# Optimization experiments

Hardware: AMD Instinct MI355X
Metric: run time of the kernel (lower is better)

Reference implementation:

```python
import jax, jax.numpy as jnp
import numpy as np

EPS = 1e-12  # F.normalize default eps

def _l2norm(v):
    # torch F.normalize: v / max(||v||, eps)
    n = jnp.sqrt(jnp.sum(v * v, axis=-1, keepdims=True))
    return v / jnp.maximum(n, EPS)

def setup_inputs() -> dict:
    key = jax.random.key(0)
    k1, k2, k3 = jax.random.split(key, 3)
    bn, cn, d = 8192, 16384, 512
    x = jax.random.normal(k1, (bn, d), dtype=jnp.float32)
    positive = jax.random.normal(k2, (bn, d), dtype=jnp.float32)
    negative = jax.random.normal(k3, (cn, d), dtype=jnp.float32)
    return {"x": x, "positive": positive, "negative": negative}

def reference(x, positive, negative):
    # normalize x and positive explicitly (as in the torch code);
    # cosine_similarity(x_n, negative) == x_n @ normalize(negative).T since x_n is unit-norm
    xn = _l2norm(x)            # (bn, d)
    pn = _l2norm(positive)     # (bn, d)
    nn_ = _l2norm(negative)    # (cn, d)
    sim = jnp.sum(xn * pn, axis=1)                 # (bn,) positive cosine sim
    logits = jnp.einsum('bd,cd->bc', xn, nn_)      # (bn, cn) cosine sims vs negatives
    denom = jnp.sum(jnp.exp(logits), axis=1)       # (bn,) -- logits bounded in [-1,1], safe
    bn = x.shape[0]
    loss = -jnp.sum(sim - jnp.log(denom)) / bn
    return loss
```

## Files before the change

kernel.cpp:

```cpp
#include <hip/hip_runtime.h>
#include <stdint.h>

#define D 512
#define BNROWS 8192
#define CNROWS 16384
#define NPART 256

typedef __attribute__((ext_vector_type(4))) float f32x4;
typedef __attribute__((ext_vector_type(8))) __bf16 bf16x8;
typedef __attribute__((ext_vector_type(8))) short s16x8;

typedef const __attribute__((address_space(1))) unsigned int* gas_ptr;
typedef __attribute__((address_space(3))) unsigned int* las_ptr;

__device__ __forceinline__ void gload_lds16(const void* g, void* l) {
    __builtin_amdgcn_global_load_lds((gas_ptr)g, (las_ptr)l, 16, 0, 0);
}

__device__ __forceinline__ short f2bf(float f) {
    uint32_t u = __float_as_uint(f);
    uint32_t r = (u + 0x7FFFu + ((u >> 16) & 1u)) >> 16;
    return (short)r;
}

__device__ __forceinline__ float wave_reduce_add(float v) {
#pragma unroll
    for (int m = 32; m >= 1; m >>= 1) v += __shfl_xor(v, m, 64);
    return v;
}

__global__ __launch_bounds__(256) void k_norm(const float* __restrict__ x,
                                              const float* __restrict__ p,
                                              const float* __restrict__ n,
                                              short* __restrict__ xnb,
                                              short* __restrict__ nnb,
                                              float* __restrict__ sim) {
    const int wid = threadIdx.x >> 6, lane = threadIdx.x & 63;
    if (blockIdx.x < BNROWS / 4) {
        const int row = blockIdx.x * 4 + wid;
        const float* xr = x + (size_t)row * D + lane * 8;
        const float* pr = p + (size_t)row * D + lane * 8;
        f32x4 x0 = *(const f32x4*)xr, x1 = *(const f32x4*)(xr + 4);
        f32x4 p0 = *(const f32x4*)pr, p1 = *(const f32x4*)(pr + 4);
        float xx = 0.f, pp = 0.f, xp = 0.f;
#pragma unroll
        for (int j = 0; j < 4; ++j) {
            xx += x0[j] * x0[j] + x1[j] * x1[j];
            pp += p0[j] * p0[j] + p1[j] * p1[j];
            xp += x0[j] * p0[j] + x1[j] * p1[j];
        }
        xx = wave_reduce_add(xx);
        pp = wave_reduce_add(pp);
        xp = wave_reduce_add(xp);
        const float rx = 1.0f / fmaxf(sqrtf(xx), 1e-12f);
        const float rp = 1.0f / fmaxf(sqrtf(pp), 1e-12f);
        if (lane == 0) sim[row] = xp * rx * rp;
        s16x8 o;
#pragma unroll
        for (int j = 0; j < 4; ++j) {
            o[j] = f2bf(x0[j] * rx);
            o[j + 4] = f2bf(x1[j] * rx);
        }
        *(s16x8*)(xnb + (size_t)row * D + lane * 8) = o;
    } else {
        const int row = (blockIdx.x - BNROWS / 4) * 4 + wid;
        const float* nr = n + (size_t)row * D + lane * 8;
        f32x4 n0 = *(const f32x4*)nr, n1 = *(const f32x4*)(nr + 4);
        float nn = 0.f;
#pragma unroll
        for (int j = 0; j < 4; ++j) nn += n0[j] * n0[j] + n1[j] * n1[j];
        nn = wave_reduce_add(nn);
        const float rn = 1.0f / fmaxf(sqrtf(nn), 1e-12f);
        s16x8 o;
#pragma unroll
        for (int j = 0; j < 4; ++j) {
            o[j] = f2bf(n0[j] * rn);
            o[j + 4] = f2bf(n1[j] * rn);
        }
        *(s16x8*)(nnb + (size_t)row * D + lane * 8) = o;
    }
}


#define LOAD_A(buf, mh)                                                                  \
    {                                                                                    \
        _Pragma("unroll") for (int m2 = 0; m2 < 4; ++m2) _Pragma("unroll") for (int ks = \
                                                                                    0;   \
                                                                                ks < 2;  \
                                                                                ++ks)    \
            af[m2 * 2 + ks] =                                                            \
            *(const bf16x8*)(Ard[buf] + (mh)*512 + m2 * 128 + ks * 4096);                \
    }
#define LOAD_B(buf, nh)                                                                  \
    {                                                                                    \
        _Pragma("unroll") for (int n2 = 0; n2 < 2; ++n2) _Pragma("unroll") for (int ks = \
                                                                                    0;   \
                                                                                ks < 2;  \
                                                                                ++ks)    \
            bfr[((nh)*2 + n2) * 2 + ks] =                                                \
            *(const bf16x8*)(Brd[buf] + ((nh)*2 + n2) * 128 + ks * 4096);                \
    }
#define MMA(mh, nh)                                                                     \
    {                                                                                   \
        _Pragma("unroll") for (int m2 = 0; m2 < 4; ++m2)                                \
            _Pragma("unroll") for (int n2 = 0; n2 < 2; ++n2)                            \
                _Pragma("unroll") for (int ks = 0; ks < 2; ++ks) acc[(mh)*4 + m2]       \
                                                                   [(nh)*2 + n2] =     \
                __builtin_amdgcn_mfma_f32_16x16x32_bf16(af[m2 * 2 + ks],                \
                                                        bfr[((nh)*2 + n2) * 2 + ks],   \
                                                        acc[(mh)*4 + m2][(nh)*2 + n2], \
                                                        0, 0, 0);                      \
    }
#define STAGE_A(buf, h, kt)                                      \
    {                                                            \
        gload_lds16(agp[h] + (kt)*64, dstA[buf][h]);             \
        gload_lds16(agp[h] + (kt)*64 + 32, dstA[buf][h] + 4096); \
    }
#define STAGE_B(buf, h, kt)                                      \
    {                                                            \
        gload_lds16(bgp[h] + (kt)*64, dstB[buf][h]);             \
        gload_lds16(bgp[h] + (kt)*64 + 32, dstB[buf][h] + 4096); \
    }
#define BAR() __builtin_amdgcn_s_barrier()
#define LGKM0() asm volatile("s_waitcnt lgkmcnt(0)" ::: "memory")
#define PRIO1() __builtin_amdgcn_s_setprio(1)
#define PRIO0() __builtin_amdgcn_s_setprio(0)
#define VMC4() asm volatile("s_waitcnt vmcnt(4)" ::: "memory")
#define VMC0() asm volatile("s_waitcnt vmcnt(0)" ::: "memory")

#define ITER(t0, ST)                                                                 \
    {                                                                                \
         LOAD_A(0, 0); LOAD_B(0, 0); STAGE_A(1, 0, (t0) + 1);                  \
        BAR(); LGKM0(); PRIO1(); MMA(0, 0); PRIO0(); BAR();                          \
         LOAD_B(0, 1); STAGE_A(1, 1, (t0) + 1);                                \
        BAR(); LGKM0(); PRIO1(); MMA(0, 1); PRIO0(); BAR();                          \
         LOAD_A(0, 1); if (ST) STAGE_B(0, 0, (t0) + 2);                        \
        BAR(); LGKM0(); PRIO1(); MMA(1, 0); PRIO0(); BAR();                          \
         if (ST) STAGE_B(0, 1, (t0) + 2);                                      \
        BAR(); PRIO1(); MMA(1, 1); PRIO0();                                          \
        if (ST) VMC4(); else VMC0();                                                 \
        BAR();                                                                       \
         LOAD_A(1, 0); LOAD_B(1, 0); if (ST) STAGE_A(0, 0, (t0) + 2);          \
        BAR(); LGKM0(); PRIO1(); MMA(0, 0); PRIO0(); BAR();                          \
         LOAD_B(1, 1); if (ST) STAGE_A(0, 1, (t0) + 2);                        \
        BAR(); LGKM0(); PRIO1(); MMA(0, 1); PRIO0(); BAR();                          \
         LOAD_A(1, 1); if (ST) STAGE_B(1, 0, (t0) + 3);                        \
        BAR(); LGKM0(); PRIO1(); MMA(1, 0); PRIO0(); BAR();                          \
         if (ST) STAGE_B(1, 1, (t0) + 3);                                      \
        BAR(); PRIO1(); MMA(1, 1); PRIO0();                                          \
        if (ST) VMC4();                                                              \
        BAR();                                                                       \
    }

__global__ __launch_bounds__(512, 2) void k_gemm_exp(const short* __restrict__ A,
                                                     const short* __restrict__ B,
                                                     float* __restrict__ part) {
    __shared__ short lds[2][2][2][8][128][8];

    const int t = threadIdx.x;
    const int lane = t & 63, wid = t >> 6;
    const int wr = wid >> 2, wc = wid & 3;
    const int lg = lane >> 4, lm = lane & 15;
    const int blockM = blockIdx.y * 256;
    const int blockN = blockIdx.x * 256;

    const int row_s = t & 127, kg_s = t >> 7;
    const short* agp[2];
    const short* bgp[2];
    short* dstA[2][2];
    short* dstB[2][2];
#pragma unroll
    for (int h = 0; h < 2; ++h) {
        agp[h] = A + (size_t)(blockM + h * 128 + row_s) * D + kg_s * 8;
        bgp[h] = B + (size_t)(blockN + h * 128 + row_s) * D + kg_s * 8;
#pragma unroll
        for (int buf = 0; buf < 2; ++buf) {
            dstA[buf][h] = &lds[buf][0][h][kg_s][row_s][0];
            dstB[buf][h] = &lds[buf][1][h][kg_s][row_s][0];
        }
    }
    const short* Ard[2];
    const short* Brd[2];
#pragma unroll
    for (int buf = 0; buf < 2; ++buf) {
        Ard[buf] = &lds[buf][0][wr][lg][lm][0];
        Brd[buf] = &lds[buf][1][wc >> 1][lg][(wc & 1) * 64 + lm][0];
    }

    f32x4 acc[8][4];
#pragma unroll
    for (int i = 0; i < 8; ++i)
#pragma unroll
        for (int j = 0; j < 4; ++j) acc[i][j] = (f32x4){0.f, 0.f, 0.f, 0.f};

    bf16x8 af[8], bfr[8];

    STAGE_A(0, 0, 0);
    STAGE_A(0, 1, 0);
    STAGE_B(0, 0, 0);
    STAGE_B(0, 1, 0);
    STAGE_B(1, 0, 1);
    STAGE_B(1, 1, 1);
    VMC4();
    BAR();

    for (int i = 0; i < 3; ++i) {
        const int t0 = 2 * i;
        ITER(t0, 1);
    }
    ITER(6, 0);

    const int pcol = blockIdx.x * 4 + wc;
    float* prow = part + (size_t)(blockM + wr * 128) * NPART + pcol;
#pragma unroll
    for (int mi = 0; mi < 8; ++mi) {
#pragma unroll
        for (int r = 0; r < 4; ++r) {
            float s = 0.f;
#pragma unroll
            for (int ni = 0; ni < 4; ++ni) s += __expf(acc[mi][ni][r]);
            s += __shfl_xor(s, 1, 64);
            s += __shfl_xor(s, 2, 64);
            s += __shfl_xor(s, 4, 64);
            s += __shfl_xor(s, 8, 64);
            if (lm == 0) prow[(size_t)(mi * 16 + lg * 4 + r) * NPART] = s;
        }
    }
}

__global__ __launch_bounds__(256) void k_final1(const float* __restrict__ part,
                                                const float* __restrict__ sim,
                                                float* __restrict__ bterm) {
    __shared__ float red[4];
    const int wid = threadIdx.x >> 6, lane = threadIdx.x & 63;
    const int row = blockIdx.x * 4 + wid;
    f32x4 v = *(const f32x4*)(part + (size_t)row * NPART + lane * 4);
    float s = v[0] + v[1] + v[2] + v[3];
    s = wave_reduce_add(s);
    float term = 0.f;
    if (lane == 0) term = sim[row] - logf(s);
    if (lane == 0) red[wid] = term;
    __syncthreads();
    if (threadIdx.x == 0)
        bterm[blockIdx.x] = red[0] + red[1] + red[2] + red[3];
}

__global__ __launch_bounds__(256) void k_final2(const float* __restrict__ bterm,
                                                float* __restrict__ out) {
    __shared__ float red[4];
    float s = 0.f;
    for (int i = threadIdx.x; i < BNROWS / 4; i += 256) s += bterm[i];
    s = wave_reduce_add(s);
    const int wid = threadIdx.x >> 6, lane = threadIdx.x & 63;
    if (lane == 0) red[wid] = s;
    __syncthreads();
    if (threadIdx.x == 0) {
        float tot = red[0] + red[1] + red[2] + red[3];
        out[0] = -tot / (float)BNROWS;
    }
}

extern "C" void kernel_launch(void* const* d_in, const int* in_sizes, int n_in,
                              void* d_out, int out_size, void* d_ws, size_t ws_size,
                              hipStream_t stream) {
    const float* x = (const float*)d_in[0];
    const float* p = (const float*)d_in[1];
    const float* n = (const float*)d_in[2];
    char* ws = (char*)d_ws;
    short* xnb = (short*)ws;
    short* nnb = (short*)(ws + (size_t)8 * 1024 * 1024);
    float* sim = (float*)(ws + (size_t)24 * 1024 * 1024);
    float* part = (float*)(ws + (size_t)24 * 1024 * 1024 + 64 * 1024);
    float* bterm = (float*)(ws + (size_t)33 * 1024 * 1024);
    float* out = (float*)d_out;

    k_norm<<<dim3(BNROWS / 4 + CNROWS / 4), dim3(256), 0, stream>>>(x, p, n, xnb, nnb,
                                                                    sim);
    k_gemm_exp<<<dim3(CNROWS / 256, BNROWS / 256), dim3(512), 0, stream>>>(xnb, nnb,
                                                                           part);
    k_final1<<<dim3(BNROWS / 4), dim3(256), 0, stream>>>(part, sim, bterm);
    k_final2<<<dim3(1), dim3(256), 0, stream>>>(bterm, out);
}
```

Measured before the change: 283.7 us.

## Merge MMA phases to halve barriers and remap blocks for XCD locality

The GEMM inner loop now issues two MMA sub-tiles per barrier-bracketed phase instead of one. This halves the number of s_barrier round-trips and groups the LDS reads and global-to-LDS stages ahead of each pair. Separately, the block index is remapped so that consecutive dispatch IDs on the same XCD (g & 7) cover a contiguous group of N-tiles, which is meant to improve L2 reuse of the B operand. The grouped phases shorten the interleaving between loads and MMAs and may raise register pressure. The remap assumes gridDim.x is 64 and the XCD count is 8.

After: 286.9 us. Within noise of the previous version (+1.1%).

```diff
diff --git a/kernel.cpp b/kernel.cpp
--- a/kernel.cpp
+++ b/kernel.cpp
@@ -128,28 +128,28 @@
 #define VMC4() asm volatile("s_waitcnt vmcnt(4)" ::: "memory")
 #define VMC0() asm volatile("s_waitcnt vmcnt(0)" ::: "memory")
 
-#define ITER(t0, ST)                                                                 \
-    {                                                                                \
-         LOAD_A(0, 0); LOAD_B(0, 0); STAGE_A(1, 0, (t0) + 1);                  \
-        BAR(); LGKM0(); PRIO1(); MMA(0, 0); PRIO0(); BAR();                          \
-         LOAD_B(0, 1); STAGE_A(1, 1, (t0) + 1);                                \
-        BAR(); LGKM0(); PRIO1(); MMA(0, 1); PRIO0(); BAR();                          \
-         LOAD_A(0, 1); if (ST) STAGE_B(0, 0, (t0) + 2);                        \
-        BAR(); LGKM0(); PRIO1(); MMA(1, 0); PRIO0(); BAR();                          \
-         if (ST) STAGE_B(0, 1, (t0) + 2);                                      \
-        BAR(); PRIO1(); MMA(1, 1); PRIO0();                                          \
-        if (ST) VMC4(); else VMC0();                                                 \
-        BAR();                                                                       \
-         LOAD_A(1, 0); LOAD_B(1, 0); if (ST) STAGE_A(0, 0, (t0) + 2);          \
-        BAR(); LGKM0(); PRIO1(); MMA(0, 0); PRIO0(); BAR();                          \
-         LOAD_B(1, 1); if (ST) STAGE_A(0, 1, (t0) + 2);                        \
-        BAR(); LGKM0(); PRIO1(); MMA(0, 1); PRIO0(); BAR();                          \
-         LOAD_A(1, 1); if (ST) STAGE_B(1, 0, (t0) + 3);                        \
-        BAR(); LGKM0(); PRIO1(); MMA(1, 0); PRIO0(); BAR();                          \
-         if (ST) STAGE_B(1, 1, (t0) + 3);                                      \
-        BAR(); PRIO1(); MMA(1, 1); PRIO0();                                          \
-        if (ST) VMC4();                                                              \
-        BAR();                                                                       \
+#define ITER(t0, ST)                                                          \
+    {                                                                         \
+               \
+        LOAD_A(0, 0); LOAD_B(0, 0); LOAD_B(0, 1);                             \
+        STAGE_A(1, 0, (t0) + 1); STAGE_A(1, 1, (t0) + 1);                     \
+        BAR(); LGKM0(); PRIO1(); MMA(0, 0); MMA(0, 1); PRIO0(); BAR();        \
+                               \
+        LOAD_A(0, 1);                                                         \
+        if (ST) { STAGE_B(0, 0, (t0) + 2); STAGE_B(0, 1, (t0) + 2); }         \
+        BAR(); LGKM0(); PRIO1(); MMA(1, 0); MMA(1, 1); PRIO0();               \
+        if (ST) VMC4(); else VMC0();                                          \
+        BAR();                                                                \
+                             \
+        LOAD_A(1, 0); LOAD_B(1, 0); LOAD_B(1, 1);                             \
+        if (ST) { STAGE_A(0, 0, (t0) + 2); STAGE_A(0, 1, (t0) + 2); }         \
+        BAR(); LGKM0(); PRIO1(); MMA(0, 0); MMA(0, 1); PRIO0(); BAR();        \
+                             \
+        LOAD_A(1, 1);                                                         \
+        if (ST) { STAGE_B(1, 0, (t0) + 3); STAGE_B(1, 1, (t0) + 3); }         \
+        BAR(); LGKM0(); PRIO1(); MMA(1, 0); MMA(1, 1); PRIO0();               \
+        if (ST) VMC4();                                                       \
+        BAR();                                                                \
     }
 
 __global__ __launch_bounds__(512, 2) void k_gemm_exp(const short* __restrict__ A,
@@ -161,8 +161,14 @@
     const int lane = t & 63, wid = t >> 6;
     const int wr = wid >> 2, wc = wid & 3;
     const int lg = lane >> 4, lm = lane & 15;
-    const int blockM = blockIdx.y * 256;
-    const int blockN = blockIdx.x * 256;
+
+    const uint32_t g = blockIdx.x + gridDim.x * blockIdx.y;
+    const int xcd = g & 7;
+    const int r_ = g >> 3;
+    const int bx = (xcd << 3) | (r_ & 7);
+    const int by = r_ >> 3;
+    const int blockM = by * 256;
+    const int blockN = bx * 256;
 
     const int row_s = t & 127, kg_s = t >> 7;
     const short* agp[2];
@@ -210,7 +216,7 @@
     }
     ITER(6, 0);
 
-    const int pcol = blockIdx.x * 4 + wc;
+    const int pcol = bx * 4 + wc;
     float* prow = part + (size_t)(blockM + wr * 128) * NPART + pcol;
 #pragma unroll
     for (int mi = 0; mi < 8; ++mi) {
```
